# Optimization experiments

Measured on AMD Instinct MI355X. Metric: run time of the kernel, lower is better.

## Reference

```python
import jax, jax.numpy as jnp
import numpy as np

D_MODEL = 256
HIDDEN = 64
R = 1            # corr_radius
MAX_DELTA = 4.0  # max_delta_px
GROUPS = 8       # _gn_groups(64)
B, H, W = 2, 128, 128


def grid_sample_border(img, grid):
    """Bilinear grid_sample, padding_mode='border', align_corners=False.
    img: [B,C,H,W], grid: [B,Hg,Wg,2] (x,y in [-1,1]-ish). -> [B,C,Hg,Wg]"""
    Bi, C, Hi, Wi = img.shape
    x = (grid[..., 0] + 1.0) * (Wi * 0.5) - 0.5
    y = (grid[..., 1] + 1.0) * (Hi * 0.5) - 0.5
    x = jnp.clip(x, 0.0, Wi - 1.0)
    y = jnp.clip(y, 0.0, Hi - 1.0)
    x0 = jnp.floor(x); y0 = jnp.floor(y)
    wx = (x - x0)[:, None]; wy = (y - y0)[:, None]
    x0i = x0.astype(jnp.int32); y0i = y0.astype(jnp.int32)
    x1i = jnp.minimum(x0i + 1, Wi - 1); y1i = jnp.minimum(y0i + 1, Hi - 1)
    imgf = img.reshape(Bi, C, Hi * Wi)
    def gat(im, yi, xi):  # im [C,HW], yi/xi [Hg,Wg]
        return im[:, (yi * Wi + xi).reshape(-1)].reshape(C, *yi.shape)
    g = jax.vmap(gat)
    v00 = g(imgf, y0i, x0i); v01 = g(imgf, y0i, x1i)
    v10 = g(imgf, y1i, x0i); v11 = g(imgf, y1i, x1i)
    return (v00 * (1 - wx) * (1 - wy) + v01 * wx * (1 - wy)
            + v10 * (1 - wx) * wy + v11 * wx * wy)


def l2norm(x, axis):
    n = jnp.sqrt(jnp.sum(x * x, axis=axis, keepdims=True))
    return x / jnp.maximum(n, 1e-12)


def conv2d(x, w, pad):
    return jax.lax.conv_general_dilated(x, w, (1, 1), [(pad, pad), (pad, pad)],
                                        dimension_numbers=('NCHW', 'OIHW', 'NCHW'))


def group_norm(x, gamma, beta, groups=GROUPS, eps=1e-5):
    Bi, C, Hi, Wi = x.shape
    xg = x.reshape(Bi, groups, C // groups, Hi, Wi)
    mu = xg.mean(axis=(2, 3, 4), keepdims=True)
    var = xg.var(axis=(2, 3, 4), keepdims=True)
    xn = ((xg - mu) * jax.lax.rsqrt(var + eps)).reshape(Bi, C, Hi, Wi)
    return xn * gamma[None, :, None, None] + beta[None, :, None, None]


def conv_gn_gelu(x, w, g, b, pad):
    return jax.nn.gelu(group_norm(conv2d(x, w, pad), g, b), approximate=False)


def make_grid(h, w):
    xs = (jnp.arange(w, dtype=jnp.float32) + 0.5) * (2.0 / w) - 1.0
    ys = (jnp.arange(h, dtype=jnp.float32) + 0.5) * (2.0 / h) - 1.0
    gx, gy = jnp.meshgrid(xs, ys, indexing='xy')
    return jnp.stack([gx, gy], axis=-1)[None]  # [1,H,W,2]


def setup_inputs() -> dict:
    key = jax.random.key(0)
    ks = jax.random.split(key, 12)
    in_ch = D_MODEL * 3 + 2 + 1 + (2 * R + 1) ** 2  # 780
    def w(k, o, i, kh, kw):
        return (jax.random.normal(k, (o, i, kh, kw), jnp.float32)
                / np.sqrt(i * kh * kw).astype(np.float32))
    return {
        'feat_A_map': jax.random.normal(ks[0], (B, D_MODEL, H, W), jnp.float32),
        'feat_B_map': jax.random.normal(ks[1], (B, D_MODEL, H, W), jnp.float32),
        'coarse_warp': jax.random.uniform(ks[2], (B, H, W, 2), jnp.float32, -1.0, 1.0),
        'confidence': jax.random.uniform(ks[3], (B, H, W), jnp.float32),
        'enc1_w': w(ks[4], HIDDEN, in_ch, 1, 1),
        'gn1_g': jnp.ones(HIDDEN, jnp.float32), 'gn1_b': jnp.zeros(HIDDEN, jnp.float32),
        'enc2_w': w(ks[5], HIDDEN, HIDDEN, 3, 3),
        'gn2_g': jnp.ones(HIDDEN, jnp.float32), 'gn2_b': jnp.zeros(HIDDEN, jnp.float32),
        'enc3_w': w(ks[6], HIDDEN, HIDDEN, 3, 3),
        'gn3_g': jnp.ones(HIDDEN, jnp.float32), 'gn3_b': jnp.zeros(HIDDEN, jnp.float32),
        'delta_w': w(ks[7], 2, HIDDEN, 3, 3) * 0.01, 'delta_b': jnp.zeros(2, jnp.float32),
        'conf_w': w(ks[8], 1, HIDDEN, 3, 3) * 0.01, 'conf_b': jnp.zeros(1, jnp.float32),
    }


def reference(feat_A_map, feat_B_map, coarse_warp, confidence,
              enc1_w, gn1_g, gn1_b, enc2_w, gn2_g, gn2_b, enc3_w, gn3_g, gn3_b,
              delta_w, delta_b, conf_w, conf_b):
    cw = jnp.clip(jnp.nan_to_num(coarse_warp, nan=0.0, posinf=1.5, neginf=-1.5), -1.5, 1.5)
    route = jax.lax.stop_gradient(cw)  # detached routing warp
    warped_B = grid_sample_border(feat_B_map, route)
    src = make_grid(H, W)
    disp = jnp.transpose(cw - src, (0, 3, 1, 2))  # [B,2,H,W]
    conf = jnp.clip(jnp.nan_to_num(confidence, nan=0.0, posinf=1.0, neginf=0.0), 0.0, 1.0)
    conf_chw = conf[:, None]
    # warp-aware correlation over (2R+1)^2 offsets, vectorized via vmap
    fa_n = l2norm(jnp.nan_to_num(feat_A_map, nan=0.0, posinf=0.0, neginf=0.0), axis=1)
    fb = jnp.nan_to_num(feat_B_map, nan=0.0, posinf=0.0, neginf=0.0)
    offs = jnp.asarray([[2.0 * dx / W, 2.0 * dy / H]
                        for dy in range(-R, R + 1) for dx in range(-R, R + 1)],
                       dtype=jnp.float32)  # [K,2]
    grids = jnp.clip(jnp.nan_to_num(route[None] + offs[:, None, None, None, :],
                                    nan=0.0, posinf=1.5, neginf=-1.5), -1.5, 1.5)
    sampled = jax.vmap(grid_sample_border, in_axes=(None, 0))(fb, grids)  # [K,B,C,H,W]
    corr = jnp.transpose(jnp.sum(fa_n[None] * l2norm(sampled, axis=2), axis=2),
                         (1, 0, 2, 3))  # [B,K,H,W]
    x = jnp.concatenate([feat_A_map, warped_B, jnp.abs(feat_A_map - warped_B),
                         disp, conf_chw, corr], axis=1)
    h = conv_gn_gelu(x, enc1_w, gn1_g, gn1_b, 0)
    h = conv_gn_gelu(h, enc2_w, gn2_g, gn2_b, 1)
    h = conv_gn_gelu(h, enc3_w, gn3_g, gn3_b, 1)
    delta_raw = jnp.transpose(jnp.tanh(conv2d(h, delta_w, 1)
                                       + delta_b[None, :, None, None]), (0, 2, 3, 1))
    scale = jnp.asarray([2.0 * MAX_DELTA / W, 2.0 * MAX_DELTA / H], jnp.float32)
    fine_warp = jnp.clip(jnp.nan_to_num(route + delta_raw * scale,
                                        nan=0.0, posinf=1.5, neginf=-1.5), -1.5, 1.5)
    conf_delta = (conv2d(h, conf_w, 1) + conf_b[None, :, None, None])[:, 0]
    p = jnp.clip(conf, 1e-4, 1.0 - 1e-4)
    base_logit = jnp.log(p) - jnp.log1p(-p)
    refined_logits = base_logit + 0.5 * conf_delta
    refined_conf = jnp.clip(jax.nn.sigmoid(refined_logits), 0.0, 1.0)
    return (fine_warp, refined_conf, refined_logits)
```

## Files before the change

### kernel.cpp

```cpp
#include <hip/hip_runtime.h>
#include <hip/hip_bf16.h>
#include <math.h>

#define B_ 2
#define H_ 128
#define W_ 128
#define C_ 256
#define HID 64
#define PIX_PER (H_*W_)
#define NPIX (B_*PIX_PER)
#define K1STEPS 25
#define K3STEPS 18
#define SROW 264

using f32x4 = __attribute__((ext_vector_type(4))) float;
using s16x8 = __attribute__((ext_vector_type(8))) short;
using u16x2 = __attribute__((ext_vector_type(2))) unsigned short;
using u16x4 = __attribute__((ext_vector_type(4))) unsigned short;
using u16x8 = __attribute__((ext_vector_type(8))) unsigned short;

__device__ __forceinline__ float bf2f(unsigned short u) {
    return __uint_as_float(((unsigned)u) << 16);
}
__device__ __forceinline__ unsigned short f2bf(float f) {
    unsigned u = __float_as_uint(f);
    u += 0x7FFFu + ((u >> 16) & 1u);
    return (unsigned short)(u >> 16);
}
__device__ __forceinline__ float clean15(float v) {
    if (v != v) v = 0.f;
    return fminf(fmaxf(v, -1.5f), 1.5f);
}
__device__ __forceinline__ float clean01(float v) {
    if (v != v) v = 0.f;
    return fminf(fmaxf(v, 0.f), 1.f);
}

__global__ __launch_bounds__(256) void k_transpose(const float* __restrict__ A,
                                                   const float* __restrict__ Bm,
                                                   unsigned short* __restrict__ faT,
                                                   unsigned short* __restrict__ fbT,
                                                   const float* __restrict__ w1,
                                                   const float* __restrict__ w2,
                                                   const float* __restrict__ w3,
                                                   unsigned short* __restrict__ p1,
                                                   unsigned short* __restrict__ p2,
                                                   unsigned short* __restrict__ p3)
{
    if (blockIdx.z == 4) {
        if (blockIdx.y != 0 || blockIdx.x >= 61) return;
        int t = blockIdx.x * 256 + threadIdx.x;
        if (t < 6400) {
            int lane = t & 63, nt = (t >> 6) & 3, ks = t >> 8;
            int n = nt * 16 + (lane & 15);
            int kb = ks * 32 + 8 * (lane >> 4);
#pragma unroll
            for (int j = 0; j < 8; j++) {
                int k = kb + j;
                p1[(size_t)t * 8 + j] = (k < 780) ? f2bf(w1[(size_t)n * 780 + k]) : (unsigned short)0;
            }
        } else if (t < 6400 + 2 * 4608) {
            int which = (t - 6400) / 4608;
            int idx = (t - 6400) % 4608;
            const float* w = which ? w3 : w2;
            unsigned short* p = which ? p3 : p2;
            int lane = idx & 63, nt = (idx >> 6) & 3, ks = idx >> 8;
            int n = nt * 16 + (lane & 15);
            int tap = ks >> 1;
            int ky = tap / 3, kx = tap % 3;
#pragma unroll
            for (int j = 0; j < 8; j++) {
                int c = (ks & 1) * 32 + 8 * (lane >> 4) + j;
                p[(size_t)idx * 8 + j] = f2bf(w[(((size_t)n * 64 + c) * 3 + ky) * 3 + kx]);
            }
        }
        return;
    }
    __shared__ float tile[32][33];
    int hw0 = blockIdx.x * 32;
    int c0  = blockIdx.y * 32;
    int z   = blockIdx.z;
    int b   = z >> 1;
    const float* src = (z & 1) ? Bm : A;
    unsigned short* dst = (z & 1) ? fbT : faT;
    int tx = threadIdx.x & 31, ty = threadIdx.x >> 5;
    const float* s = src + ((size_t)b * C_ + c0) * (size_t)PIX_PER + hw0;
#pragma unroll
    for (int i = 0; i < 32; i += 8) {
        float v = s[(size_t)(ty + i) * PIX_PER + tx];
        if (!isfinite(v)) v = 0.f;
        tile[ty + i][tx] = v;
    }
    __syncthreads();
    unsigned short* d = dst + ((size_t)b * PIX_PER + hw0) * C_ + c0;
    int pr = threadIdx.x & 7;
    int hw = threadIdx.x >> 3;
    u16x4 o;
#pragma unroll
    for (int j = 0; j < 4; j++) o[j] = f2bf(tile[4 * pr + j][hw]);
    *(u16x4*)(d + (size_t)hw * C_ + 4 * pr) = o;
}

__global__ __launch_bounds__(256) void k_sample(const float* __restrict__ cw,
                                                const float* __restrict__ confp,
                                                const unsigned short* __restrict__ faT,
                                                const unsigned short* __restrict__ fbT,
                                                unsigned short* __restrict__ wbbuf,
                                                unsigned short* __restrict__ tail)
{
    __shared__ unsigned short S[4][17 * SROW];
    __shared__ float CT[4][16 * 20 + 4];
    int lane = threadIdx.x & 63;
    int wv = threadIdx.x >> 6;
    int wid = blockIdx.x * 4 + wv;
    int b = wid >> 14, y = (wid >> 7) & 127, x = wid & 127;

    float gx = clean15(cw[(size_t)wid * 2 + 0]);
    float gy = clean15(cw[(size_t)wid * 2 + 1]);
    float conf = clean01(confp[wid]);

    float pxu = (gx + 1.f) * 64.f - 0.5f;
    float pyu = (gy + 1.f) * 64.f - 0.5f;
    float x0f = floorf(pxu), y0f = floorf(pyu);
    float wx = pxu - x0f, wy = pyu - y0f;
    int x0 = (int)x0f, y0 = (int)y0f;
    int co[4], ro[4];
#pragma unroll
    for (int k = 0; k < 4; k++) {
        co[k] = min(max(x0 - 1 + k, 0), 127) << 8;
        ro[k] = min(max(y0 - 1 + k, 0), 127) << 15;
    }
    const unsigned short* fbP = fbT + ((size_t)b << 22);

    int h = lane >> 5, lo = lane & 31;
    u16x8 stg[8];
#pragma unroll
    for (int i = 0; i < 8; i++) {
        int rr = ro[i >> 1];
        int cc = h ? co[((i & 1) << 1) + 1] : co[(i & 1) << 1];
        stg[i] = *(const u16x8*)(fbP + rr + cc + lo * 8);
    }
    u16x8 stfa;
    if (h == 0) stfa = *(const u16x8*)(faT + (size_t)wid * C_ + lo * 8);

    unsigned short* Sw = &S[wv][0];
#pragma unroll
    for (int i = 0; i < 8; i++)
        *(u16x8*)(Sw + (2 * i + h) * SROW + lo * 8) = stg[i];
    if (h == 0) *(u16x8*)(Sw + 16 * SROW + lo * 8) = stfa;

    int q = lane & 15;
    int tA = (q == 0) ? 16 : q - 1;
    int koff = (lane >> 4) * 8;
    const unsigned short* pA = Sw + tA * SROW + koff;
    const unsigned short* pB = Sw + q * SROW + koff;
    f32x4 acc = {0.f, 0.f, 0.f, 0.f};
#pragma unroll
    for (int ks = 0; ks < 8; ks++) {
        s16x8 av = *(const s16x8*)(pA + ks * 32);
        s16x8 bv = *(const s16x8*)(pB + ks * 32);
        acc = __builtin_amdgcn_mfma_f32_16x16x32_bf16(av, bv, acc, 0, 0, 0);
    }
    *(f32x4*)&CT[wv][q * 20 + (lane >> 4) * 4] = acc;

    float w00 = (1.f - wx) * (1.f - wy), w01 = wx * (1.f - wy);
    float w10 = (1.f - wx) * wy,         w11 = wx * wy;
    u16x4 v5  = *(const u16x4*)(Sw + 5 * SROW + lane * 4);
    u16x4 v6  = *(const u16x4*)(Sw + 6 * SROW + lane * 4);
    u16x4 v9  = *(const u16x4*)(Sw + 9 * SROW + lane * 4);
    u16x4 v10 = *(const u16x4*)(Sw + 10 * SROW + lane * 4);
    u16x4 v15 = *(const u16x4*)(Sw + 15 * SROW + lane * 4);
    u16x4 vfa = *(const u16x4*)(Sw + 16 * SROW + lane * 4);
    float fa2p = 0.f, t152p = 0.f;
    u16x4 wbo;
#pragma unroll
    for (int i = 0; i < 4; i++) {
        float s = w00 * bf2f(v5[i]) + w01 * bf2f(v6[i])
                + w10 * bf2f(v9[i]) + w11 * bf2f(v10[i]);
        wbo[i] = f2bf(s);
        float fv = bf2f(vfa[i]), tv = bf2f(v15[i]);
        fa2p  += fv * fv;
        t152p += tv * tv;
    }
    *(u16x4*)(wbbuf + (size_t)wid * C_ + lane * 4) = wbo;
#pragma unroll
    for (int m = 1; m < 64; m <<= 1) {
        fa2p  += __shfl_xor(fa2p, m);
        t152p += __shfl_xor(t152p, m);
    }

    if (lane < 32) {
        float outv = 0.f;
        if (lane == 0)      outv = gx - (((float)x + 0.5f) * 0.015625f - 1.f);
        else if (lane == 1) outv = gy - (((float)y + 0.5f) * 0.015625f - 1.f);
        else if (lane == 2) outv = conf;
        else if (lane < 12) {
            int j = lane - 3;
            int jd = j / 3, jm = j - jd * 3;
            int m00 = jd * 4 + jm;
            const float* Cw = &CT[wv][0];
            float D00 = Cw[m00 * 20], D01 = Cw[(m00 + 1) * 20];
            float D10 = Cw[(m00 + 4) * 20], D11 = Cw[(m00 + 5) * 20];
            float dot = w00 * D00 + w01 * D01 + w10 * D10 + w11 * D11;
#define GR(a, b) Cw[(b) * 20 + (a) + 1]
            float g11 = (j == 8) ? t152p : GR(m00 + 5, m00 + 5);
            float s2 = w00 * w00 * GR(m00, m00) + w01 * w01 * GR(m00 + 1, m00 + 1)
                     + w10 * w10 * GR(m00 + 4, m00 + 4) + w11 * w11 * g11
                     + 2.f * (w00 * w01 * GR(m00, m00 + 1) + w00 * w10 * GR(m00, m00 + 4)
                            + w00 * w11 * GR(m00, m00 + 5) + w01 * w10 * GR(m00 + 1, m00 + 4)
                            + w01 * w11 * GR(m00 + 1, m00 + 5) + w10 * w11 * GR(m00 + 4, m00 + 5));
#undef GR
            outv = dot * rsqrtf(fmaxf(fa2p, 1e-24f)) * rsqrtf(fmaxf(s2, 1e-24f));
        }
        tail[(size_t)wid * 32 + lane] = f2bf(outv);
    }
}

__device__ __forceinline__ void gn_epilogue(const f32x4 acc[4], float* lds,
                                            float* __restrict__ pbuf, int bid,
                                            int la, int lb, int wv)
{
    int d = la >> 3;
    int slot = wv * 32 + lb * 8 + (la & 7);
#pragma unroll
    for (int nt = 0; nt < 4; nt++) {
        float s  = acc[nt][0] + acc[nt][1] + acc[nt][2] + acc[nt][3];
        float s2 = acc[nt][0] * acc[nt][0] + acc[nt][1] * acc[nt][1]
                 + acc[nt][2] * acc[nt][2] + acc[nt][3] * acc[nt][3];
        int g = nt * 2 + d;
        lds[(g * 128 + slot) * 2 + 0] = s;
        lds[(g * 128 + slot) * 2 + 1] = s2;
    }
    __syncthreads();
    int tid = threadIdx.x;
    int g = tid >> 5, i = tid & 31;
    float s  = lds[(g * 128 + i) * 2]     + lds[(g * 128 + i + 32) * 2]
             + lds[(g * 128 + i + 64) * 2] + lds[(g * 128 + i + 96) * 2];
    float s2 = lds[(g * 128 + i) * 2 + 1]     + lds[(g * 128 + i + 32) * 2 + 1]
             + lds[(g * 128 + i + 64) * 2 + 1] + lds[(g * 128 + i + 96) * 2 + 1];
#pragma unroll
    for (int m = 1; m < 32; m <<= 1) { s += __shfl_xor(s, m); s2 += __shfl_xor(s2, m); }
    if (i == 0) {
        pbuf[(bid * 8 + g) * 2]     = s;
        pbuf[(bid * 8 + g) * 2 + 1] = s2;
    }
}

__global__ __launch_bounds__(256) void k_gemm1(const unsigned short* __restrict__ faT,
                                               const unsigned short* __restrict__ wbbuf,
                                               const unsigned short* __restrict__ tail,
                                               const unsigned short* __restrict__ pack,
                                               unsigned short* __restrict__ hpre,
                                               float* __restrict__ pbuf)
{
    __shared__ float lds[8 * 128 * 2];
    int wave = (blockIdx.x * 256 + threadIdx.x) >> 6;
    int lane = threadIdx.x & 63;
    int la = lane & 15, lb = lane >> 4;
    int row = wave * 16 + la;
    const unsigned short* fa_row = faT   + (size_t)row * C_ + lb * 8;
    const unsigned short* wb_row = wbbuf + (size_t)row * C_ + lb * 8;
    f32x4 acc[4] = {{0,0,0,0},{0,0,0,0},{0,0,0,0},{0,0,0,0}};

#pragma unroll
    for (int ks = 0; ks < 8; ks++) {
        s16x8 a = *(const s16x8*)(fa_row + ks * 32);
#pragma unroll
        for (int nt = 0; nt < 4; nt++)
            acc[nt] = __builtin_amdgcn_mfma_f32_16x16x32_bf16(a,
                *(const s16x8*)(pack + ((size_t)(ks * 4 + nt) * 64 + lane) * 8), acc[nt], 0, 0, 0);
    }
#pragma unroll
    for (int ks = 0; ks < 8; ks++) {
        s16x8 a = *(const s16x8*)(wb_row + ks * 32);
#pragma unroll
        for (int nt = 0; nt < 4; nt++)
            acc[nt] = __builtin_amdgcn_mfma_f32_16x16x32_bf16(a,
                *(const s16x8*)(pack + ((size_t)((ks + 8) * 4 + nt) * 64 + lane) * 8), acc[nt], 0, 0, 0);
    }
#pragma unroll
    for (int ks = 0; ks < 8; ks++) {
        u16x8 av = *(const u16x8*)(fa_row + ks * 32);
        u16x8 bv = *(const u16x8*)(wb_row + ks * 32);
        s16x8 a;
#pragma unroll
        for (int j = 0; j < 8; j++)
            a[j] = (short)f2bf(fabsf(bf2f(av[j]) - bf2f(bv[j])));
#pragma unroll
        for (int nt = 0; nt < 4; nt++)
            acc[nt] = __builtin_amdgcn_mfma_f32_16x16x32_bf16(a,
                *(const s16x8*)(pack + ((size_t)((ks + 16) * 4 + nt) * 64 + lane) * 8), acc[nt], 0, 0, 0);
    }
    {
        s16x8 a = *(const s16x8*)(tail + (size_t)row * 32 + lb * 8);
#pragma unroll
        for (int nt = 0; nt < 4; nt++)
            acc[nt] = __builtin_amdgcn_mfma_f32_16x16x32_bf16(a,
                *(const s16x8*)(pack + ((size_t)(24 * 4 + nt) * 64 + lane) * 8), acc[nt], 0, 0, 0);
    }

    int orow = wave * 16 + lb * 4;
#pragma unroll
    for (int nt = 0; nt < 4; nt++)
#pragma unroll
        for (int r = 0; r < 4; r++)
            hpre[(size_t)(orow + r) * HID + nt * 16 + la] = f2bf(acc[nt][r]);

    gn_epilogue(acc, lds, pbuf, blockIdx.x, la, lb, (threadIdx.x >> 6));
}

__global__ __launch_bounds__(256) void k_conv3(const unsigned short* __restrict__ hin,
                                               const unsigned short* __restrict__ pack,
                                               unsigned short* __restrict__ hpre,
                                               float* __restrict__ pbuf)
{
    __shared__ float lds[8 * 128 * 2];
    int wave = (blockIdx.x * 256 + threadIdx.x) >> 6;
    int lane = threadIdx.x & 63;
    int la = lane & 15, lb = lane >> 4;
    int b = wave >> 10, y = (wave >> 3) & 127, xb = (wave & 7) * 16;
    int xx = xb + la;
    f32x4 acc[4] = {{0,0,0,0},{0,0,0,0},{0,0,0,0},{0,0,0,0}};
#pragma unroll
    for (int ks = 0; ks < K3STEPS; ks++) {
        int tap = ks >> 1;
        int yy = y + tap / 3 - 1;
        int xq = xx + tap % 3 - 1;
        s16x8 a = {0,0,0,0,0,0,0,0};
        if ((unsigned)yy < 128u && (unsigned)xq < 128u)
            a = *(const s16x8*)(hin + ((size_t)((b * 128 + yy) * 128 + xq)) * HID
                                + (ks & 1) * 32 + lb * 8);
#pragma unroll
        for (int nt = 0; nt < 4; nt++)
            acc[nt] = __builtin_amdgcn_mfma_f32_16x16x32_bf16(a,
                *(const s16x8*)(pack + ((size_t)(ks * 4 + nt) * 64 + lane) * 8), acc[nt], 0, 0, 0);
    }
    int orow = wave * 16 + lb * 4;
#pragma unroll
    for (int nt = 0; nt < 4; nt++)
#pragma unroll
        for (int r = 0; r < 4; r++)
            hpre[(size_t)(orow + r) * HID + nt * 16 + la] = f2bf(acc[nt][r]);

    gn_epilogue(acc, lds, pbuf, blockIdx.x, la, lb, (threadIdx.x >> 6));
}

__global__ __launch_bounds__(256) void k_gnapply(const unsigned short* __restrict__ hpre,
                                                 const float* __restrict__ gamma,
                                                 const float* __restrict__ beta,
                                                 const float* __restrict__ pbuf,
                                                 unsigned short* __restrict__ hn)
{
    int pix0 = blockIdx.x * 32;
    int b = pix0 >> 14;
    __shared__ float sm[16];
    {
        int g = threadIdx.x >> 5, i = threadIdx.x & 31;
        float s = 0.f, s2 = 0.f;
#pragma unroll
        for (int k = 0; k < 8; k++) {
            int bid = b * 256 + i + k * 32;
            s  += pbuf[(bid * 8 + g) * 2];
            s2 += pbuf[(bid * 8 + g) * 2 + 1];
        }
#pragma unroll
        for (int m = 1; m < 32; m <<= 1) { s += __shfl_xor(s, m); s2 += __shfl_xor(s2, m); }
        if (i == 0) {
            const float inv = 1.f / 131072.f;
            float mean = s * inv;
            float var = fmaxf(s2 * inv - mean * mean, 0.f);
            sm[g * 2] = mean;
            sm[g * 2 + 1] = rsqrtf(var + 1e-5f);
        }
    }
    __syncthreads();
    int t = blockIdx.x * 256 + threadIdx.x;
    int pix = t >> 3, g = t & 7;
    float mean = sm[g * 2], rstd = sm[g * 2 + 1];
    u16x8 v = *(const u16x8*)(hpre + (size_t)pix * HID + g * 8);
    u16x8 o;
#pragma unroll
    for (int i = 0; i < 8; i++) {
        int c = g * 8 + i;
        float xn = (bf2f(v[i]) - mean) * rstd * gamma[c] + beta[c];
        float ge = 0.5f * xn * (1.f + erff(xn * 0.70710678118654752f));
        o[i] = f2bf(ge);
    }
    *(u16x8*)(hn + (size_t)pix * HID + g * 8) = o;
}

__global__ __launch_bounds__(256) void k_gnfinal(const unsigned short* __restrict__ hpre,
                                                 const float* __restrict__ gamma,
                                                 const float* __restrict__ beta,
                                                 const float* __restrict__ pbuf,
                                                 const float* __restrict__ cw,
                                                 const float* __restrict__ confp,
                                                 const float* __restrict__ dw,
                                                 const float* __restrict__ db,
                                                 const float* __restrict__ cwgt,
                                                 const float* __restrict__ cb,
                                                 float* __restrict__ out)
{
    __shared__ unsigned short hnT[100 * 68];
    __shared__ float wds[1154];
    __shared__ float wcs[577];
    __shared__ float sm[16];
    int tid = threadIdx.x;
    int bid = blockIdx.x;
    int b = bid >> 8;
    int tile = bid & 255;
    int ty0 = (tile >> 4) << 3, tx0 = (tile & 15) << 3;

    for (int i = tid; i < 1152; i += 256) wds[i] = dw[i];
    for (int i = tid; i < 576; i += 256) wcs[i] = cwgt[i];
    if (tid == 0) { wds[1152] = db[0]; wds[1153] = db[1]; wcs[576] = cb[0]; }

    {
        int g = tid >> 5, i = tid & 31;
        float s = 0.f, s2 = 0.f;
#pragma unroll
        for (int k = 0; k < 8; k++) {
            int pb = b * 256 + i + k * 32;
            s  += pbuf[(pb * 8 + g) * 2];
            s2 += pbuf[(pb * 8 + g) * 2 + 1];
        }
#pragma unroll
        for (int m = 1; m < 32; m <<= 1) { s += __shfl_xor(s, m); s2 += __shfl_xor(s2, m); }
        if (i == 0) {
            const float inv = 1.f / 131072.f;
            float mean = s * inv;
            float var = fmaxf(s2 * inv - mean * mean, 0.f);
            sm[g * 2] = mean;
            sm[g * 2 + 1] = rsqrtf(var + 1e-5f);
        }
    }
    __syncthreads();

#pragma unroll
    for (int pass = 0; pass < 4; pass++) {
        int idx = pass * 256 + tid;
        if (idx < 800) {
            int slot = idx >> 3, c8 = idx & 7;
            int py = slot / 10, px = slot - py * 10;
            int gy = ty0 + py - 1, gx = tx0 + px - 1;
            u16x8 o = {0, 0, 0, 0, 0, 0, 0, 0};
            if ((unsigned)gy < 128u && (unsigned)gx < 128u) {
                int gpix = (b << 14) + (gy << 7) + gx;
                u16x8 v = *(const u16x8*)(hpre + (size_t)gpix * HID + c8 * 8);
                float mean = sm[c8 * 2], rstd = sm[c8 * 2 + 1];
#pragma unroll
                for (int i = 0; i < 8; i++) {
                    int c = c8 * 8 + i;
                    float xn = (bf2f(v[i]) - mean) * rstd * gamma[c] + beta[c];
                    float ge = 0.5f * xn * (1.f + erff(xn * 0.70710678118654752f));
                    o[i] = f2bf(ge);
                }
            }
            *(u16x8*)(&hnT[slot * 68 + c8 * 8]) = o;
        }
    }
    __syncthreads();

    int p = tid >> 2, part = tid & 3;
    int py = (p >> 3) + 1, px = (p & 7) + 1;
    float d0 = 0.f, d1 = 0.f, c0 = 0.f;
#pragma unroll
    for (int ky = 0; ky < 3; ky++)
#pragma unroll
        for (int kx = 0; kx < 3; kx++) {
            const unsigned short* hp = &hnT[((py + ky - 1) * 10 + (px + kx - 1)) * 68];
            int widx = ky * 3 + kx;
#pragma unroll
            for (int cc = 0; cc < 2; cc++) {
                int c8 = part * 2 + cc;
                u16x8 v = *(const u16x8*)(hp + c8 * 8);
#pragma unroll
                for (int i = 0; i < 8; i++) {
                    float f = bf2f(v[i]);
                    int c = c8 * 8 + i;
                    d0 += f * wds[c * 9 + widx];
                    d1 += f * wds[576 + c * 9 + widx];
                    c0 += f * wcs[c * 9 + widx];
                }
            }
        }
#pragma unroll
    for (int m = 1; m < 4; m <<= 1) {
        d0 += __shfl_xor(d0, m);
        d1 += __shfl_xor(d1, m);
        c0 += __shfl_xor(c0, m);
    }
    if (part == 0) {
        int pix = (b << 14) + ((ty0 + py - 1) << 7) + (tx0 + px - 1);
        d0 = tanhf(d0 + wds[1152]);
        d1 = tanhf(d1 + wds[1153]);
        c0 += wcs[576];

        float gx = clean15(cw[(size_t)pix * 2 + 0]);
        float gy = clean15(cw[(size_t)pix * 2 + 1]);
        float fwx = fminf(fmaxf(gx + d0 * 0.0625f, -1.5f), 1.5f);
        float fwy = fminf(fmaxf(gy + d1 * 0.0625f, -1.5f), 1.5f);

        float conf = clean01(confp[pix]);
        float pp = fminf(fmaxf(conf, 1e-4f), 1.f - 1e-4f);
        float bl = logf(pp) - log1pf(-pp);
        float rl = bl + 0.5f * c0;
        float rc = fminf(fmaxf(1.f / (1.f + expf(-rl)), 0.f), 1.f);

        out[(size_t)pix * 2 + 0] = fwx;
        out[(size_t)pix * 2 + 1] = fwy;
        out[(size_t)NPIX * 2 + pix] = rc;
        out[(size_t)NPIX * 2 + NPIX + pix] = rl;
    }
}

extern "C" void kernel_launch(void* const* d_in, const int* in_sizes, int n_in,
                              void* d_out, int out_size, void* d_ws, size_t ws_size,
                              hipStream_t stream)
{
    const float* feat_A = (const float*)d_in[0];
    const float* feat_B = (const float*)d_in[1];
    const float* cw     = (const float*)d_in[2];
    const float* conf   = (const float*)d_in[3];
    const float* w1     = (const float*)d_in[4];
    const float* g1     = (const float*)d_in[5];
    const float* b1     = (const float*)d_in[6];
    const float* w2     = (const float*)d_in[7];
    const float* g2     = (const float*)d_in[8];
    const float* b2     = (const float*)d_in[9];
    const float* w3     = (const float*)d_in[10];
    const float* g3     = (const float*)d_in[11];
    const float* b3     = (const float*)d_in[12];
    const float* dw     = (const float*)d_in[13];
    const float* db     = (const float*)d_in[14];
    const float* cwgt   = (const float*)d_in[15];
    const float* cb     = (const float*)d_in[16];
    float* out = (float*)d_out;

    char* w = (char*)d_ws;
    size_t o = 0;
    unsigned short* faT  = (unsigned short*)(w + o); o += (size_t)NPIX * C_ * 2;
    unsigned short* fbT  = (unsigned short*)(w + o); o += (size_t)NPIX * C_ * 2;
    unsigned short* wbb  = (unsigned short*)(w + o); o += (size_t)NPIX * C_ * 2;
    unsigned short* tail = (unsigned short*)(w + o); o += (size_t)NPIX * 32 * 2;
    unsigned short* hpre = (unsigned short*)(w + o); o += (size_t)NPIX * HID * 2;
    unsigned short* hnA  = (unsigned short*)(w + o); o += (size_t)NPIX * HID * 2;
    unsigned short* hnB  = (unsigned short*)(w + o); o += (size_t)NPIX * HID * 2;
    unsigned short* p1   = (unsigned short*)(w + o); o += (size_t)K1STEPS * 4 * 64 * 8 * 2;
    unsigned short* p2   = (unsigned short*)(w + o); o += (size_t)K3STEPS * 4 * 64 * 8 * 2;
    unsigned short* p3   = (unsigned short*)(w + o); o += (size_t)K3STEPS * 4 * 64 * 8 * 2;
    float* pbuf = (float*)(w + o);

    k_transpose<<<dim3(PIX_PER / 32, C_ / 32, 5), 256, 0, stream>>>(feat_A, feat_B, faT, fbT,
                                                                    w1, w2, w3, p1, p2, p3);
    k_sample<<<NPIX / 4, 256, 0, stream>>>(cw, conf, faT, fbT, wbb, tail);

    k_gemm1<<<(NPIX / 16) / 4, 256, 0, stream>>>(faT, wbb, tail, p1, hpre, pbuf);
    k_gnapply<<<NPIX / 32, 256, 0, stream>>>(hpre, g1, b1, pbuf, hnA);

    k_conv3<<<(NPIX / 16) / 4, 256, 0, stream>>>(hnA, p2, hpre, pbuf);
    k_gnapply<<<NPIX / 32, 256, 0, stream>>>(hpre, g2, b2, pbuf, hnB);

    k_conv3<<<(NPIX / 16) / 4, 256, 0, stream>>>(hnB, p3, hpre, pbuf);
    k_gnfinal<<<512, 256, 0, stream>>>(hpre, g3, b3, pbuf, cw, conf,
                                       dw, db, cwgt, cb, out);
}
```

Measured before the change: 137.3 us.

## Fuse GroupNorm+GELU apply into 3x3 conv via 8x8 LDS halo tiles

Removes the separate k_gnapply launches. Each conv block now loads an 8x8 spatial tile plus a one-pixel halo of the previous pre-norm activations, applies GroupNorm and exact GELU while staging into LDS, and feeds the MFMA from LDS. The 3x3 neighbourhood reads no longer go to global memory, and one full write plus read of the normalized activations per layer is avoided. In exchange, halo pixels are normalized redundantly (100 vs 64 pixels per tile) and the output writes now scatter over a 2D tile. Separate per-layer partial-stat buffers avoid read/write conflicts on pbuf.

```diff
diff --git a/kernel.cpp b/kernel.cpp
--- a/kernel.cpp
+++ b/kernel.cpp
@@ -309,59 +309,31 @@
     gn_epilogue(acc, lds, pbuf, blockIdx.x, la, lb, (threadIdx.x >> 6));
 }
 
-__global__ __launch_bounds__(256) void k_conv3(const unsigned short* __restrict__ hin,
-                                               const unsigned short* __restrict__ pack,
-                                               unsigned short* __restrict__ hpre,
-                                               float* __restrict__ pbuf)
-{
-    __shared__ float lds[8 * 128 * 2];
-    int wave = (blockIdx.x * 256 + threadIdx.x) >> 6;
-    int lane = threadIdx.x & 63;
-    int la = lane & 15, lb = lane >> 4;
-    int b = wave >> 10, y = (wave >> 3) & 127, xb = (wave & 7) * 16;
-    int xx = xb + la;
-    f32x4 acc[4] = {{0,0,0,0},{0,0,0,0},{0,0,0,0},{0,0,0,0}};
-#pragma unroll
-    for (int ks = 0; ks < K3STEPS; ks++) {
-        int tap = ks >> 1;
-        int yy = y + tap / 3 - 1;
-        int xq = xx + tap % 3 - 1;
-        s16x8 a = {0,0,0,0,0,0,0,0};
-        if ((unsigned)yy < 128u && (unsigned)xq < 128u)
-            a = *(const s16x8*)(hin + ((size_t)((b * 128 + yy) * 128 + xq)) * HID
-                                + (ks & 1) * 32 + lb * 8);
-#pragma unroll
-        for (int nt = 0; nt < 4; nt++)
-            acc[nt] = __builtin_amdgcn_mfma_f32_16x16x32_bf16(a,
-                *(const s16x8*)(pack + ((size_t)(ks * 4 + nt) * 64 + lane) * 8), acc[nt], 0, 0, 0);
-    }
-    int orow = wave * 16 + lb * 4;
-#pragma unroll
-    for (int nt = 0; nt < 4; nt++)
-#pragma unroll
-        for (int r = 0; r < 4; r++)
-            hpre[(size_t)(orow + r) * HID + nt * 16 + la] = f2bf(acc[nt][r]);
-
-    gn_epilogue(acc, lds, pbuf, blockIdx.x, la, lb, (threadIdx.x >> 6));
-}
-
-__global__ __launch_bounds__(256) void k_gnapply(const unsigned short* __restrict__ hpre,
-                                                 const float* __restrict__ gamma,
-                                                 const float* __restrict__ beta,
-                                                 const float* __restrict__ pbuf,
-                                                 unsigned short* __restrict__ hn)
-{
-    int pix0 = blockIdx.x * 32;
-    int b = pix0 >> 14;
+__global__ __launch_bounds__(256) void k_convgn(const unsigned short* __restrict__ hin,
+                                                const float* __restrict__ gamma,
+                                                const float* __restrict__ beta,
+                                                const float* __restrict__ pbin,
+                                                const unsigned short* __restrict__ pack,
+                                                unsigned short* __restrict__ hout,
+                                                float* __restrict__ pbout)
+{
+    __shared__ unsigned short T[8 * 100 * 8];
+    __shared__ float eplds[8 * 128 * 2];
     __shared__ float sm[16];
+    int tid = threadIdx.x;
+    int bid = blockIdx.x;
+    int b = bid >> 8;
+    int tile = bid & 255;
+    int ty0 = (tile >> 4) << 3, tx0 = (tile & 15) << 3;
+
     {
-        int g = threadIdx.x >> 5, i = threadIdx.x & 31;
+        int g = tid >> 5, i = tid & 31;
         float s = 0.f, s2 = 0.f;
 #pragma unroll
         for (int k = 0; k < 8; k++) {
-            int bid = b * 256 + i + k * 32;
-            s  += pbuf[(bid * 8 + g) * 2];
-            s2 += pbuf[(bid * 8 + g) * 2 + 1];
+            int pb = b * 256 + i + k * 32;
+            s  += pbin[(pb * 8 + g) * 2];
+            s2 += pbin[(pb * 8 + g) * 2 + 1];
         }
 #pragma unroll
         for (int m = 1; m < 32; m <<= 1) { s += __shfl_xor(s, m); s2 += __shfl_xor(s2, m); }
@@ -374,19 +346,60 @@
         }
     }
     __syncthreads();
-    int t = blockIdx.x * 256 + threadIdx.x;
-    int pix = t >> 3, g = t & 7;
-    float mean = sm[g * 2], rstd = sm[g * 2 + 1];
-    u16x8 v = *(const u16x8*)(hpre + (size_t)pix * HID + g * 8);
-    u16x8 o;
-#pragma unroll
-    for (int i = 0; i < 8; i++) {
-        int c = g * 8 + i;
-        float xn = (bf2f(v[i]) - mean) * rstd * gamma[c] + beta[c];
-        float ge = 0.5f * xn * (1.f + erff(xn * 0.70710678118654752f));
-        o[i] = f2bf(ge);
-    }
-    *(u16x8*)(hn + (size_t)pix * HID + g * 8) = o;
+
+#pragma unroll
+    for (int pass = 0; pass < 4; pass++) {
+        int idx = pass * 256 + tid;
+        if (idx < 800) {
+            int c8 = idx & 7, slot = idx >> 3;
+            int py = slot / 10, px = slot - py * 10;
+            int gy = ty0 + py - 1, gx = tx0 + px - 1;
+            u16x8 o = {0, 0, 0, 0, 0, 0, 0, 0};
+            if ((unsigned)gy < 128u && (unsigned)gx < 128u) {
+                int gpix = (b << 14) + (gy << 7) + gx;
+                u16x8 v = *(const u16x8*)(hin + (size_t)gpix * HID + c8 * 8);
+                float mean = sm[c8 * 2], rstd = sm[c8 * 2 + 1];
+#pragma unroll
+                for (int i = 0; i < 8; i++) {
+                    int c = c8 * 8 + i;
+                    float xn = (bf2f(v[i]) - mean) * rstd * gamma[c] + beta[c];
+                    o[i] = f2bf(0.5f * xn * (1.f + erff(xn * 0.70710678118654752f)));
+                }
+            }
+            *(u16x8*)(&T[(c8 * 100 + slot) * 8]) = o;
+        }
+    }
+    __syncthreads();
+
+    int lane = tid & 63, wv = tid >> 6;
+    int la = lane & 15, lb = lane >> 4;
+    int ay = la >> 3, ax = la & 7;
+    f32x4 acc[4] = {{0,0,0,0},{0,0,0,0},{0,0,0,0},{0,0,0,0}};
+#pragma unroll
+    for (int ks = 0; ks < K3STEPS; ks++) {
+        int tap = ks >> 1;
+        int dy = tap / 3, dx = tap - dy * 3;
+        int c8 = (ks & 1) * 4 + lb;
+        int py = wv * 2 + ay + dy;
+        int px = ax + dx;
+        s16x8 a = *(const s16x8*)(&T[(c8 * 100 + py * 10 + px) * 8]);
+#pragma unroll
+        for (int nt = 0; nt < 4; nt++)
+            acc[nt] = __builtin_amdgcn_mfma_f32_16x16x32_bf16(a,
+                *(const s16x8*)(pack + ((size_t)(ks * 4 + nt) * 64 + lane) * 8), acc[nt], 0, 0, 0);
+    }
+
+#pragma unroll
+    for (int nt = 0; nt < 4; nt++)
+#pragma unroll
+        for (int r = 0; r < 4; r++) {
+            int po = lb * 4 + r;
+            int yy = ty0 + wv * 2 + (po >> 3);
+            int xx = tx0 + (po & 7);
+            hout[((size_t)((b << 14) + (yy << 7) + xx)) * HID + nt * 16 + la] = f2bf(acc[nt][r]);
+        }
+
+    gn_epilogue(acc, eplds, pbout, bid, la, lb, wv);
 }
 
 __global__ __launch_bounds__(256) void k_gnfinal(const unsigned short* __restrict__ hpre,
@@ -543,25 +556,22 @@
     unsigned short* fbT  = (unsigned short*)(w + o); o += (size_t)NPIX * C_ * 2;
     unsigned short* wbb  = (unsigned short*)(w + o); o += (size_t)NPIX * C_ * 2;
     unsigned short* tail = (unsigned short*)(w + o); o += (size_t)NPIX * 32 * 2;
-    unsigned short* hpre = (unsigned short*)(w + o); o += (size_t)NPIX * HID * 2;
-    unsigned short* hnA  = (unsigned short*)(w + o); o += (size_t)NPIX * HID * 2;
-    unsigned short* hnB  = (unsigned short*)(w + o); o += (size_t)NPIX * HID * 2;
+    unsigned short* hA   = (unsigned short*)(w + o); o += (size_t)NPIX * HID * 2;
+    unsigned short* hB   = (unsigned short*)(w + o); o += (size_t)NPIX * HID * 2;
     unsigned short* p1   = (unsigned short*)(w + o); o += (size_t)K1STEPS * 4 * 64 * 8 * 2;
     unsigned short* p2   = (unsigned short*)(w + o); o += (size_t)K3STEPS * 4 * 64 * 8 * 2;
     unsigned short* p3   = (unsigned short*)(w + o); o += (size_t)K3STEPS * 4 * 64 * 8 * 2;
-    float* pbuf = (float*)(w + o);
+    float* pbuf1 = (float*)(w + o); o += 512 * 8 * 2 * 4;
+    float* pbuf2 = (float*)(w + o); o += 512 * 8 * 2 * 4;
+    float* pbuf3 = (float*)(w + o); o += 512 * 8 * 2 * 4;
 
     k_transpose<<<dim3(PIX_PER / 32, C_ / 32, 5), 256, 0, stream>>>(feat_A, feat_B, faT, fbT,
                                                                     w1, w2, w3, p1, p2, p3);
     k_sample<<<NPIX / 4, 256, 0, stream>>>(cw, conf, faT, fbT, wbb, tail);
 
-    k_gemm1<<<(NPIX / 16) / 4, 256, 0, stream>>>(faT, wbb, tail, p1, hpre, pbuf);
-    k_gnapply<<<NPIX / 32, 256, 0, stream>>>(hpre, g1, b1, pbuf, hnA);
-
-    k_conv3<<<(NPIX / 16) / 4, 256, 0, stream>>>(hnA, p2, hpre, pbuf);
-    k_gnapply<<<NPIX / 32, 256, 0, stream>>>(hpre, g2, b2, pbuf, hnB);
-
-    k_conv3<<<(NPIX / 16) / 4, 256, 0, stream>>>(hnB, p3, hpre, pbuf);
-    k_gnfinal<<<512, 256, 0, stream>>>(hpre, g3, b3, pbuf, cw, conf,
+    k_gemm1<<<(NPIX / 16) / 4, 256, 0, stream>>>(faT, wbb, tail, p1, hA, pbuf1);
+    k_convgn<<<512, 256, 0, stream>>>(hA, g1, b1, pbuf1, p2, hB, pbuf2);
+    k_convgn<<<512, 256, 0, stream>>>(hB, g2, b2, pbuf2, p3, hA, pbuf3);
+    k_gnfinal<<<512, 256, 0, stream>>>(hA, g3, b3, pbuf3, cw, conf,
                                        dw, db, cwgt, cb, out);
 }
```

Result: faster. 126.0 us, median of 2 (-8.3%).
